# Kernel tuning notes

Hardware: AMD Instinct MI355X
Metric: run time of the kernel (lower is better)

Reference implementation:

```python
import jax, jax.numpy as jnp
import numpy as np

N_USERS = 100000
N_ITEMS = 50000
N_ENTITIES = 150000
N_EDGES = 2000000
NNZ = 1000000
CHANNEL = 64
N_HOPS = 2
TEMPERATURE = 0.2
PDIST_EPS = 1e-6   # torch.nn.PairwiseDistance default eps (added to the diff)
NORM_EPS = 1e-12   # F.normalize default eps


def setup_inputs() -> dict:
    key = jax.random.key(0)
    ks = jax.random.split(key, 8)
    return {
        "user_emb": jax.random.normal(ks[0], (N_USERS, CHANNEL), dtype=jnp.float32),
        "entity_emb": jax.random.normal(ks[1], (N_ENTITIES, CHANNEL), dtype=jnp.float32),
        "weight": jax.random.normal(ks[2], (20, CHANNEL), dtype=jnp.float32),
        "edge_index": jax.random.randint(ks[3], (2, N_EDGES), 0, N_ENTITIES, dtype=jnp.int64) if jax.config.jax_enable_x64 else jax.random.randint(ks[3], (2, N_EDGES), 0, N_ENTITIES, dtype=jnp.int32),
        "edge_type": jax.random.randint(ks[4], (N_EDGES,), 0, 20, dtype=jnp.int32),
        "inter_user": jax.random.randint(ks[5], (NNZ,), 0, N_USERS, dtype=jnp.int32),
        "inter_item": jax.random.randint(ks[6], (NNZ,), 0, N_ITEMS, dtype=jnp.int32),
        "inter_vals": jax.random.uniform(ks[7], (NNZ,), dtype=jnp.float32),
    }


def _l2_normalize(x):
    # F.normalize(x, p=2, dim=1): x / max(||x||, eps)
    n = jnp.sqrt(jnp.sum(x * x, axis=-1, keepdims=True))
    return x / jnp.maximum(n, NORM_EPS)


def _aggregate(entity_emb, head, tail, inter_user, inter_item, inter_vals):
    n_entities = entity_emb.shape[0]
    # scatter_mean over KG edges: mean of tail embeddings per head entity
    neigh = entity_emb[tail]                                   # [E, C]
    summed = jax.ops.segment_sum(neigh, head, num_segments=n_entities)
    cnt = jax.ops.segment_sum(jnp.ones((head.shape[0],), entity_emb.dtype), head,
                              num_segments=n_entities)
    entity_agg = summed / jnp.maximum(cnt, 1.0)[:, None]       # [n_entities, C]

    items = entity_agg[:N_ITEMS]                               # [n_items, C]
    g_items = items[inter_item]                                # [nnz, C]
    # user_mean = interact_map @ entity_agg[:n_items]  (sparse mm via segment_sum)
    user_mean = jax.ops.segment_sum(inter_vals[:, None] * g_items, inter_user,
                                    num_segments=N_USERS)      # [n_users, C]
    # pairwise L2 distance per interaction edge
    diff = g_items - user_mean[inter_user] + PDIST_EPS
    score = jnp.sqrt(jnp.sum(diff * diff, axis=-1)) / TEMPERATURE   # [nnz]
    # sparse softmax over each user row
    row_max = jax.ops.segment_max(score, inter_user, num_segments=N_USERS)
    e = jnp.exp(score - row_max[inter_user])
    denom = jax.ops.segment_sum(e, inter_user, num_segments=N_USERS)
    soft = e / denom[inter_user]                               # [nnz]
    # user_agg = soft_score_mat @ entity_agg[:n_items]
    user_agg = jax.ops.segment_sum(soft[:, None] * g_items, inter_user,
                                   num_segments=N_USERS)       # [n_users, C]
    return user_agg, entity_agg


def reference(user_emb, entity_emb, weight, edge_index, edge_type,
              inter_user, inter_item, inter_vals):
    # GraphConv.forward with mess_dropout=False, node_dropout=False (deterministic)
    head, tail = edge_index[0], edge_index[1]
    user_res, entity_res = user_emb, entity_emb
    u, ent = user_emb, entity_emb
    for _ in range(N_HOPS):
        u, ent = _aggregate(ent, head, tail, inter_user, inter_item, inter_vals)
        ent = _l2_normalize(ent)
        u = _l2_normalize(u)
        entity_res = entity_res + ent
        user_res = user_res + u
    return user_res, entity_res
```

## Files before the change

kernel.cpp:

```cpp
#include <hip/hip_runtime.h>

#define N_USERS   100000
#define N_ITEMS   50000
#define N_ENT     150000
#define N_EDGES   2000000
#define NNZ       1000000
#define CH        64

#define CB_SHIFT  9
#define CB_SIZE   512
#define NB_E      ((N_ENT   + CB_SIZE - 1) >> CB_SHIFT)
#define NB_U      ((N_USERS + CB_SIZE - 1) >> CB_SHIFT)
#define A_CHUNK   4096
#define UCACHE    32

#define NBLK_CNT   512
#define NBLK_CONV  ((N_ENT * 16 + 255) / 256)
#define NBLK_BS_E  ((N_EDGES + A_CHUNK - 1) / A_CHUNK)
#define NBLK_BS_U  ((NNZ + A_CHUNK - 1) / A_CHUNK)
#define GB_GATHER  (N_ENT / 4)
#define GB_USER    (N_USERS / 4)

typedef __fp16 h2v __attribute__((ext_vector_type(2)));

__device__ __forceinline__ h2v h2z() { h2v z = {(__fp16)0.f, (__fp16)0.f}; return z; }
__device__ __forceinline__ h2v pk(float a, float b) { return __builtin_amdgcn_cvt_pkrtz(a, b); }
__device__ __forceinline__ unsigned int h2u(h2v h) { return __builtin_bit_cast(unsigned int, h); }
__device__ __forceinline__ h2v u2h(unsigned int u) { return __builtin_bit_cast(h2v, u); }
__device__ __forceinline__ float fdot2f(h2v a, h2v b, float c) {
    return __builtin_amdgcn_fdot2(a, b, c, false);
}

template<int CTRL>
__device__ __forceinline__ float dpp_mov(float x) {
    return __builtin_bit_cast(float, __builtin_amdgcn_update_dpp(
        0, __builtin_bit_cast(int, x), CTRL, 0xF, 0xF, true));
}
template<int CTRL>
__device__ __forceinline__ unsigned dpp_mov_u(unsigned x) {
    return (unsigned)__builtin_amdgcn_update_dpp(0, (int)x, CTRL, 0xF, 0xF, true);
}
__device__ __forceinline__ float red8(float x) {
    x += dpp_mov<0xB1>(x);
    x += dpp_mov<0x4E>(x);
    x += dpp_mov<0x141>(x);
    return x;
}
__device__ __forceinline__ h2v grpadd8(h2v a) {
    return a + u2h(dpp_mov_u<0x128>(h2u(a)));
}


__device__ __forceinline__ void coarse_count_f(const int* __restrict__ key, int n,
                                               unsigned int* __restrict__ gcnt, int nb,
                                               unsigned int* h, int bid, int nblk) {
    for (int i = threadIdx.x; i < nb; i += blockDim.x) h[i] = 0;
    __syncthreads();
    for (int e = bid * blockDim.x + threadIdx.x; e < n; e += nblk * blockDim.x)
        atomicAdd(&h[key[e] >> CB_SHIFT], 1u);
    __syncthreads();
    for (int i = threadIdx.x; i < nb; i += blockDim.x)
        if (h[i]) atomicAdd(&gcnt[i], h[i]);
}

__global__ void build_p1(const int* __restrict__ head, const int* __restrict__ iu,
                         const float* __restrict__ entity_emb, uint2* __restrict__ E0,
                         unsigned int* __restrict__ cntE, unsigned int* __restrict__ cntU) {
    __shared__ unsigned int h[CB_SIZE];
    int bid = blockIdx.x;
    if (bid < NBLK_CNT) {
        coarse_count_f(head, N_EDGES, cntE, NB_E, h, bid, NBLK_CNT);
    } else if (bid < 2 * NBLK_CNT) {
        coarse_count_f(iu, NNZ, cntU, NB_U, h, bid - NBLK_CNT, NBLK_CNT);
    } else {
        int i = (bid - 2 * NBLK_CNT) * 256 + threadIdx.x;
        if (i < N_ENT * 16) {
            float4 a = ((const float4*)entity_emb)[i];
            E0[i] = make_uint2(h2u(pk(a.x, a.y)), h2u(pk(a.z, a.w)));
        }
    }
}

__device__ __forceinline__ void coarse_scan_f(const unsigned int* __restrict__ gcnt,
                                              unsigned int* __restrict__ base,
                                              unsigned int* __restrict__ cursor, int nb,
                                              unsigned int* s) {
    int t = threadIdx.x;
    unsigned int v = (t < nb) ? gcnt[t] : 0u;
    s[t] = v;
    __syncthreads();
    for (int off = 1; off < 512; off <<= 1) {
        unsigned int u = 0;
        if (t >= off) u = s[t - off];
        __syncthreads();
        if (t >= off) s[t] += u;
        __syncthreads();
    }
    if (t < nb) { base[t] = s[t] - v; cursor[t] = s[t] - v; }
    if (t == nb) base[t] = s[nb - 1];
}

__global__ void build_p2(const unsigned int* __restrict__ cntE, unsigned int* __restrict__ baseE,
                         unsigned int* __restrict__ curE,
                         const unsigned int* __restrict__ cntU, unsigned int* __restrict__ baseU,
                         unsigned int* __restrict__ curU) {
    __shared__ unsigned int s[512];
    if (blockIdx.x == 0) coarse_scan_f(cntE, baseE, curE, NB_E, s);
    else                 coarse_scan_f(cntU, baseU, curU, NB_U, s);
}

__device__ __forceinline__ void binscat_ent_f(const int* __restrict__ head,
                                              const int* __restrict__ tail,
                                              unsigned int* __restrict__ cursor,
                                              unsigned int* __restrict__ binned,
                                              unsigned int* h, unsigned int* bb, int bid) {
    int lo = bid * A_CHUNK;
    int hi = min(lo + A_CHUNK, N_EDGES);
    for (int i = threadIdx.x; i < NB_E; i += blockDim.x) h[i] = 0;
    __syncthreads();
    for (int e = lo + threadIdx.x; e < hi; e += blockDim.x)
        atomicAdd(&h[head[e] >> CB_SHIFT], 1u);
    __syncthreads();
    for (int i = threadIdx.x; i < NB_E; i += blockDim.x) {
        unsigned int c = h[i];
        bb[i] = c ? atomicAdd(&cursor[i], c) : 0u;
        h[i] = 0;
    }
    __syncthreads();
    for (int e = lo + threadIdx.x; e < hi; e += blockDim.x) {
        int hd = head[e];
        int b = hd >> CB_SHIFT;
        unsigned int r = atomicAdd(&h[b], 1u);
        unsigned int local = (unsigned int)hd & (CB_SIZE - 1);
        binned[bb[b] + r] = (local << 18) | (unsigned int)tail[e];
    }
}

__device__ __forceinline__ void binscat_user_f(const int* __restrict__ iu,
                                               const int* __restrict__ ii,
                                               const float* __restrict__ iv,
                                               unsigned int* __restrict__ cursor,
                                               unsigned int* __restrict__ binned,
                                               float* __restrict__ binnedv,
                                               unsigned int* h, unsigned int* bb, int bid) {
    int lo = bid * A_CHUNK;
    int hi = min(lo + A_CHUNK, NNZ);
    for (int i = threadIdx.x; i < NB_U; i += blockDim.x) h[i] = 0;
    __syncthreads();
    for (int e = lo + threadIdx.x; e < hi; e += blockDim.x)
        atomicAdd(&h[iu[e] >> CB_SHIFT], 1u);
    __syncthreads();
    for (int i = threadIdx.x; i < NB_U; i += blockDim.x) {
        unsigned int c = h[i];
        bb[i] = c ? atomicAdd(&cursor[i], c) : 0u;
        h[i] = 0;
    }
    __syncthreads();
    for (int e = lo + threadIdx.x; e < hi; e += blockDim.x) {
        int u = iu[e];
        int b = u >> CB_SHIFT;
        unsigned int r = atomicAdd(&h[b], 1u);
        unsigned int slot = bb[b] + r;
        unsigned int local = (unsigned int)u & (CB_SIZE - 1);
        binned[slot] = (local << 16) | (unsigned int)ii[e];
        binnedv[slot] = iv[e];
    }
}

__global__ void build_p3e(const int* __restrict__ head, const int* __restrict__ tail,
                          unsigned int* __restrict__ curE, unsigned int* __restrict__ binnedE) {
    __shared__ unsigned int h[NB_E];
    __shared__ unsigned int bb[NB_E];
    binscat_ent_f(head, tail, curE, binnedE, h, bb, blockIdx.x);
}

__device__ __forceinline__ void build_ent_f(const unsigned int* __restrict__ base,
                                            const unsigned int* __restrict__ binned,
                                            int* __restrict__ col,
                                            unsigned int* __restrict__ row_start,
                                            unsigned int* h, unsigned int* ex,
                                            unsigned int* pairs, int b) {
    unsigned int s0 = base[b], s1 = base[b + 1];
    int t = threadIdx.x;
    h[2 * t] = 0; h[2 * t + 1] = 0;
    __syncthreads();
    for (unsigned int j = s0 + t; j < s1; j += 256)
        atomicAdd(&h[binned[j] >> 18], 1u);
    __syncthreads();
    unsigned int a0 = h[2 * t], a1 = h[2 * t + 1];
    pairs[t] = a0 + a1;
    __syncthreads();
    for (int off = 1; off < 256; off <<= 1) {
        unsigned int u = 0;
        if (t >= off) u = pairs[t - off];
        __syncthreads();
        if (t >= off) pairs[t] += u;
        __syncthreads();
    }
    unsigned int pe = pairs[t] - (a0 + a1);
    ex[2 * t] = pe;
    ex[2 * t + 1] = pe + a0;
    __syncthreads();
    int keybase = b << CB_SHIFT;
    #pragma unroll
    for (int k = 0; k < 2; ++k) {
        int i = 2 * t + k;
        int key = keybase + i;
        if (key < N_ENT) row_start[key] = s0 + ex[i];
    }
    if (b == 0 && t == 0) row_start[N_ENT] = base[NB_E];
    __syncthreads();
    h[2 * t] = 0; h[2 * t + 1] = 0;
    __syncthreads();
    for (unsigned int j = s0 + t; j < s1; j += 256) {
        unsigned int p = binned[j];
        unsigned int local = p >> 18;
        unsigned int r = atomicAdd(&h[local], 1u);
        col[s0 + ex[local] + r] = (int)(p & 0x3FFFFu);
    }
}

__device__ __forceinline__ void build_user_f(const unsigned int* __restrict__ base,
                                             const unsigned int* __restrict__ binned,
                                             const float* __restrict__ binnedv,
                                             int2* __restrict__ upair,
                                             unsigned int* __restrict__ u_row_start,
                                             unsigned int* h, unsigned int* ex,
                                             unsigned int* pairs, int b) {
    unsigned int s0 = base[b], s1 = base[b + 1];
    int t = threadIdx.x;
    h[2 * t] = 0; h[2 * t + 1] = 0;
    __syncthreads();
    for (unsigned int j = s0 + t; j < s1; j += 256)
        atomicAdd(&h[binned[j] >> 16], 1u);
    __syncthreads();
    unsigned int a0 = h[2 * t], a1 = h[2 * t + 1];
    pairs[t] = a0 + a1;
    __syncthreads();
    for (int off = 1; off < 256; off <<= 1) {
        unsigned int u = 0;
        if (t >= off) u = pairs[t - off];
        __syncthreads();
        if (t >= off) pairs[t] += u;
        __syncthreads();
    }
    unsigned int pe = pairs[t] - (a0 + a1);
    ex[2 * t] = pe;
    ex[2 * t + 1] = pe + a0;
    __syncthreads();
    int keybase = b << CB_SHIFT;
    #pragma unroll
    for (int k = 0; k < 2; ++k) {
        int i = 2 * t + k;
        int key = keybase + i;
        if (key < N_USERS) u_row_start[key] = s0 + ex[i];
    }
    if (b == 0 && t == 0) u_row_start[N_USERS] = base[NB_U];
    __syncthreads();
    h[2 * t] = 0; h[2 * t + 1] = 0;
    __syncthreads();
    for (unsigned int j = s0 + t; j < s1; j += 256) {
        unsigned int p = binned[j];
        float v = binnedv[j];
        unsigned int local = p >> 16;
        unsigned int r = atomicAdd(&h[local], 1u);
        upair[s0 + ex[local] + r] = make_int2((int)(p & 0xFFFFu), __float_as_int(v));
    }
}

__global__ void build_p3u_p4e(const int* __restrict__ iu, const int* __restrict__ ii,
                              const float* __restrict__ iv, unsigned int* __restrict__ curU,
                              unsigned int* __restrict__ binnedU, float* __restrict__ binnedUV,
                              const unsigned int* __restrict__ baseE,
                              const unsigned int* __restrict__ binnedE,
                              int* __restrict__ col, unsigned int* __restrict__ row_start) {
    __shared__ unsigned int h[CB_SIZE];
    __shared__ unsigned int ex[CB_SIZE];
    __shared__ unsigned int pairs[256];
    if (blockIdx.x < NBLK_BS_U)
        binscat_user_f(iu, ii, iv, curU, binnedU, binnedUV, h, ex , blockIdx.x);
    else
        build_ent_f(baseE, binnedE, col, row_start, h, ex, pairs, blockIdx.x - NBLK_BS_U);
}


__device__ __forceinline__ void gather_fin_row(int row, int lane,
        const uint4* __restrict__ entb, const unsigned int* __restrict__ row_start,
        const int* __restrict__ col,
        uint4* __restrict__ ent_out, uint4* __restrict__ items_out,
        const float* __restrict__ base_ent, const uint4* __restrict__ v1tab,
        float* __restrict__ out_ent, int mode) {
    int grp = lane >> 3;
    int t   = lane & 7;
    unsigned int s0 = row_start[row];
    unsigned int s1 = row_start[row + 1];

    h2v a0 = h2z(), a1 = h2z(), a2 = h2z(), a3 = h2z();
    unsigned int j = s0 + grp;
    for (; j + 8 < s1; j += 16) {
        uint4 x0 = entb[(size_t)col[j]     * 8 + t];
        uint4 x1 = entb[(size_t)col[j + 8] * 8 + t];
        a0 += u2h(x0.x) + u2h(x1.x);
        a1 += u2h(x0.y) + u2h(x1.y);
        a2 += u2h(x0.z) + u2h(x1.z);
        a3 += u2h(x0.w) + u2h(x1.w);
    }
    if (j < s1) {
        uint4 x = entb[(size_t)col[j] * 8 + t];
        a0 += u2h(x.x); a1 += u2h(x.y); a2 += u2h(x.z); a3 += u2h(x.w);
    }
    a0 = grpadd8(a0); a1 = grpadd8(a1); a2 = grpadd8(a2); a3 = grpadd8(a3);
    #pragma unroll
    for (int m = 16; m <= 32; m <<= 1) {
        a0 += u2h(__shfl_xor(h2u(a0), m, 64));
        a1 += u2h(__shfl_xor(h2u(a1), m, 64));
        a2 += u2h(__shfl_xor(h2u(a2), m, 64));
        a3 += u2h(__shfl_xor(h2u(a3), m, 64));
    }
    float inv = 1.0f / fmaxf((float)(s1 - s0), 1.0f);
    float m0 = (float)a0[0] * inv, m1 = (float)a0[1] * inv;
    float m2 = (float)a1[0] * inv, m3 = (float)a1[1] * inv;
    float m4 = (float)a2[0] * inv, m5 = (float)a2[1] * inv;
    float m6 = (float)a3[0] * inv, m7 = (float)a3[1] * inv;

    float sq = m0*m0 + m1*m1 + m2*m2 + m3*m3 + m4*m4 + m5*m5 + m6*m6 + m7*m7;
    sq = red8(sq);
    float invn = 1.0f / fmaxf(sqrtf(sq), 1e-12f);

    if (grp == 0) {
        size_t o = (size_t)row * 8 + t;
        if (row < N_ITEMS)
            items_out[o] = make_uint4(h2u(pk(m0, m1)), h2u(pk(m2, m3)),
                                      h2u(pk(m4, m5)), h2u(pk(m6, m7)));
        if (mode == 0) {
            ent_out[o] = make_uint4(h2u(pk(m0*invn, m1*invn)), h2u(pk(m2*invn, m3*invn)),
                                    h2u(pk(m4*invn, m5*invn)), h2u(pk(m6*invn, m7*invn)));
        } else {
            size_t fo = (size_t)row * 16 + 2 * t;
            float4 c0 = ((const float4*)base_ent)[fo];
            float4 c1 = ((const float4*)base_ent)[fo + 1];
            uint4 v1 = v1tab[o];
            h2v p0 = u2h(v1.x), p1 = u2h(v1.y), p2 = u2h(v1.z), p3 = u2h(v1.w);
            ((float4*)out_ent)[fo]     = make_float4(c0.x + (float)p0[0] + m0*invn,
                                                     c0.y + (float)p0[1] + m1*invn,
                                                     c0.z + (float)p1[0] + m2*invn,
                                                     c0.w + (float)p1[1] + m3*invn);
            ((float4*)out_ent)[fo + 1] = make_float4(c1.x + (float)p2[0] + m4*invn,
                                                     c1.y + (float)p2[1] + m5*invn,
                                                     c1.z + (float)p3[0] + m6*invn,
                                                     c1.w + (float)p3[1] + m7*invn);
        }
    }
}

template<int NS>
__device__ __forceinline__ void user_fast_path(
        unsigned int s0, unsigned int deg, int grp, int t,
        const uint4* __restrict__ itemsb, const int2* __restrict__ up,
        float& l, h2v& ac0, h2v& ac1, h2v& ac2, h2v& ac3) {
    const float SC = 5.0f * 1.44269504f;
    uint4 r[NS];
    float vw[NS];
    #pragma unroll
    for (int k = 0; k < NS; ++k) {
        unsigned int slot = (unsigned int)grp + 8u * k;
        if (slot < deg) {
            int2 p = up[s0 + slot];
            r[k] = itemsb[(size_t)p.x * 8 + t];
            vw[k] = __int_as_float(p.y);
        } else {
            r[k] = make_uint4(0u, 0u, 0u, 0u);
            vw[k] = 0.0f;
        }
    }
    h2v um0 = h2z(), um1 = h2z(), um2 = h2z(), um3 = h2z();
    #pragma unroll
    for (int k = 0; k < NS; ++k) {
        h2v v2 = pk(vw[k], vw[k]);
        um0 += v2 * u2h(r[k].x); um1 += v2 * u2h(r[k].y);
        um2 += v2 * u2h(r[k].z); um3 += v2 * u2h(r[k].w);
    }
    um0 = grpadd8(um0); um1 = grpadd8(um1); um2 = grpadd8(um2); um3 = grpadd8(um3);
    #pragma unroll
    for (int m = 16; m <= 32; m <<= 1) {
        um0 += u2h(__shfl_xor(h2u(um0), m, 64));
        um1 += u2h(__shfl_xor(h2u(um1), m, 64));
        um2 += u2h(__shfl_xor(h2u(um2), m, 64));
        um3 += u2h(__shfl_xor(h2u(um3), m, 64));
    }
    float scv[NS];
    float mloc = -1e30f;
    #pragma unroll
    for (int k = 0; k < NS; ++k) {
        unsigned int slot = (unsigned int)grp + 8u * k;
        h2v d0 = u2h(r[k].x) - um0, d1 = u2h(r[k].y) - um1;
        h2v d2 = u2h(r[k].z) - um2, d3 = u2h(r[k].w) - um3;
        float sq = fdot2f(d3, d3, fdot2f(d2, d2, fdot2f(d1, d1, fdot2f(d0, d0, 0.0f))));
        sq = red8(sq);
        float sc = sqrtf(sq) * SC;
        scv[k] = (slot < deg) ? sc : -1e30f;
        mloc = fmaxf(mloc, scv[k]);
    }
    mloc = fmaxf(mloc, dpp_mov<0x128>(mloc));
    float M = fmaxf(mloc, __shfl_xor(mloc, 16, 64));
    M = fmaxf(M, __shfl_xor(M, 32, 64));
    #pragma unroll
    for (int k = 0; k < NS; ++k) {
        float e = exp2f(scv[k] - M);
        l += e;
        h2v e2 = pk(e, e);
        ac0 += e2 * u2h(r[k].x); ac1 += e2 * u2h(r[k].y);
        ac2 += e2 * u2h(r[k].z); ac3 += e2 * u2h(r[k].w);
    }
}

__device__ __forceinline__ void fused_user_row(int row, int lane, uint4 (*cw)[8],
        const uint4* __restrict__ itemsb, const unsigned int* __restrict__ u_row_start,
        const int2* __restrict__ up, const float* __restrict__ base_user,
        float* __restrict__ out_user) {
    int grp = lane >> 3;
    int t   = lane & 7;
    unsigned int s0 = u_row_start[row];
    unsigned int s1 = u_row_start[row + 1];
    unsigned int deg = s1 - s0;

    const float SC = 5.0f * 1.44269504f;
    float l = 0.0f;
    h2v ac0 = h2z(), ac1 = h2z(), ac2 = h2z(), ac3 = h2z();

    if (__builtin_expect(deg <= 16, 1)) {
        user_fast_path<2>(s0, deg, grp, t, itemsb, up, l, ac0, ac1, ac2, ac3);
    } else if (deg <= UCACHE) {
        user_fast_path<4>(s0, deg, grp, t, itemsb, up, l, ac0, ac1, ac2, ac3);
    } else {
        h2v um0 = h2z(), um1 = h2z(), um2 = h2z(), um3 = h2z();
        for (unsigned int j = s0 + grp; j < s1; j += 8) {
            int2 p = up[j];
            uint4 r = itemsb[(size_t)p.x * 8 + t];
            int slot = (int)(j - s0);
            if (slot < UCACHE) cw[slot][t] = r;
            float v = __int_as_float(p.y);
            h2v v2 = pk(v, v);
            um0 += v2 * u2h(r.x); um1 += v2 * u2h(r.y);
            um2 += v2 * u2h(r.z); um3 += v2 * u2h(r.w);
        }
        um0 = grpadd8(um0); um1 = grpadd8(um1); um2 = grpadd8(um2); um3 = grpadd8(um3);
        #pragma unroll
        for (int m = 16; m <= 32; m <<= 1) {
            um0 += u2h(__shfl_xor(h2u(um0), m, 64));
            um1 += u2h(__shfl_xor(h2u(um1), m, 64));
            um2 += u2h(__shfl_xor(h2u(um2), m, 64));
            um3 += u2h(__shfl_xor(h2u(um3), m, 64));
        }
        float m_run = -1e30f;
        for (unsigned int j = s0 + grp; j < s1; j += 8) {
            int slot = (int)(j - s0);
            uint4 r = (slot < UCACHE) ? cw[slot][t]
                                      : itemsb[(size_t)up[j].x * 8 + t];
            h2v d0 = u2h(r.x) - um0, d1 = u2h(r.y) - um1;
            h2v d2 = u2h(r.z) - um2, d3 = u2h(r.w) - um3;
            float sq = fdot2f(d3, d3, fdot2f(d2, d2, fdot2f(d1, d1, fdot2f(d0, d0, 0.0f))));
            sq = red8(sq);
            float sc = sqrtf(sq) * SC;
            if (sc > m_run) {
                float s = exp2f(m_run - sc);
                l *= s;
                h2v s2 = pk(s, s);
                ac0 *= s2; ac1 *= s2; ac2 *= s2; ac3 *= s2;
                m_run = sc;
            }
            float e = exp2f(sc - m_run);
            l += e;
            h2v e2 = pk(e, e);
            ac0 += e2 * u2h(r.x); ac1 += e2 * u2h(r.y);
            ac2 += e2 * u2h(r.z); ac3 += e2 * u2h(r.w);
        }
        float mx = fmaxf(m_run, dpp_mov<0x128>(m_run));
        float M = fmaxf(mx, __shfl_xor(mx, 16, 64));
        M = fmaxf(M, __shfl_xor(M, 32, 64));
        float wgt = (l > 0.0f) ? exp2f(m_run - M) : 0.0f;
        l *= wgt;
        h2v w2 = pk(wgt, wgt);
        ac0 *= w2; ac1 *= w2; ac2 *= w2; ac3 *= w2;
    }

    l = l + dpp_mov<0x128>(l);
    ac0 = grpadd8(ac0); ac1 = grpadd8(ac1); ac2 = grpadd8(ac2); ac3 = grpadd8(ac3);
    #pragma unroll
    for (int m = 16; m <= 32; m <<= 1) {
        l   += __shfl_xor(l, m, 64);
        ac0 += u2h(__shfl_xor(h2u(ac0), m, 64));
        ac1 += u2h(__shfl_xor(h2u(ac1), m, 64));
        ac2 += u2h(__shfl_xor(h2u(ac2), m, 64));
        ac3 += u2h(__shfl_xor(h2u(ac3), m, 64));
    }
    float invl = (l > 0.0f) ? (1.0f / l) : 0.0f;
    float u0 = (float)ac0[0] * invl, u1 = (float)ac0[1] * invl;
    float u2 = (float)ac1[0] * invl, u3 = (float)ac1[1] * invl;
    float u4 = (float)ac2[0] * invl, u5 = (float)ac2[1] * invl;
    float u6 = (float)ac3[0] * invl, u7 = (float)ac3[1] * invl;

    float sq2 = u0*u0 + u1*u1 + u2*u2 + u3*u3 + u4*u4 + u5*u5 + u6*u6 + u7*u7;
    sq2 = red8(sq2);
    float inv = 1.0f / fmaxf(sqrtf(sq2), 1e-12f);
    if (grp == 0) {
        size_t fo = (size_t)row * 16 + 2 * t;
        float4 c0 = ((const float4*)base_user)[fo];
        float4 c1 = ((const float4*)base_user)[fo + 1];
        ((float4*)out_user)[fo]     = make_float4(c0.x + u0*inv, c0.y + u1*inv,
                                                  c0.z + u2*inv, c0.w + u3*inv);
        ((float4*)out_user)[fo + 1] = make_float4(c1.x + u4*inv, c1.y + u5*inv,
                                                  c1.z + u6*inv, c1.w + u7*inv);
    }
}


__global__ void gf1_p4u_k(const uint4* __restrict__ E0,
                          const unsigned int* __restrict__ row_start,
                          const int* __restrict__ col,
                          uint4* __restrict__ E1, uint4* __restrict__ itemsA,
                          const unsigned int* __restrict__ baseU,
                          const unsigned int* __restrict__ binnedU,
                          const float* __restrict__ binnedUV,
                          int2* __restrict__ upair, unsigned int* __restrict__ u_row_start) {
    __shared__ unsigned int h[CB_SIZE];
    __shared__ unsigned int ex[CB_SIZE];
    __shared__ unsigned int pairs[256];
    int bid = blockIdx.x;
    if (bid < NB_U) {
        build_user_f(baseU, binnedU, binnedUV, upair, u_row_start, h, ex, pairs, bid);
    } else {
        int row  = (bid - NB_U) * 4 + (threadIdx.x >> 6);
        gather_fin_row(row, threadIdx.x & 63, E0, row_start, col, E1, itemsA,
                       nullptr, nullptr, nullptr, 0);
    }
}

__global__ void g2_u1_k(const uint4* __restrict__ entb,
                        const unsigned int* __restrict__ row_start,
                        const int* __restrict__ col,
                        uint4* __restrict__ items_out,
                        const float* __restrict__ entity_emb,
                        float* __restrict__ out_ent,
                        const uint4* __restrict__ itemsb1,
                        const unsigned int* __restrict__ u_row_start,
                        const int2* __restrict__ up,
                        const float* __restrict__ base_user,
                        float* __restrict__ out_user) {
    __shared__ uint4 cache[4][UCACHE][8];
    int bid = blockIdx.x;
    int g5 = bid / 5, r5 = bid - g5 * 5;
    int w    = threadIdx.x >> 6;
    int lane = threadIdx.x & 63;
    if (r5 < 3) {
        int row = (g5 * 3 + r5) * 4 + w;
        gather_fin_row(row, lane, entb, row_start, col, nullptr, items_out,
                       entity_emb, entb, out_ent, 1);
    } else {
        int row = (g5 * 2 + (r5 - 3)) * 4 + w;
        fused_user_row(row, lane, cache[w], itemsb1, u_row_start, up,
                       base_user, out_user);
    }
}

__global__ void fused_user_k(const uint4* __restrict__ itemsb,
                             const unsigned int* __restrict__ u_row_start,
                             const int2* __restrict__ up,
                             const float* __restrict__ base_user,
                             float* __restrict__ out_user) {
    __shared__ uint4 cache[4][UCACHE][8];
    int wave = (blockIdx.x * blockDim.x + threadIdx.x) >> 6;
    int w    = threadIdx.x >> 6;
    int lane = threadIdx.x & 63;
    if (wave >= N_USERS) return;
    fused_user_row(wave, lane, cache[w], itemsb, u_row_start, up, base_user, out_user);
}

extern "C" void kernel_launch(void* const* d_in, const int* in_sizes, int n_in,
                              void* d_out, int out_size, void* d_ws, size_t ws_size,
                              hipStream_t stream) {
    const float* user_emb   = (const float*)d_in[0];
    const float* entity_emb = (const float*)d_in[1];
    const int*   edge_index = (const int*)d_in[3];
    const int*   iu = (const int*)d_in[5];
    const int*   ii = (const int*)d_in[6];
    const float* iv = (const float*)d_in[7];

    float* out_user = (float*)d_out;
    float* out_ent  = out_user + (size_t)N_USERS * CH;

    uint4* E0     = (uint4*)d_ws;
    uint4* E1     = E0 + (size_t)N_ENT * 8;
    uint4* itemsA = E1 + (size_t)N_ENT * 8;
    uint4* itemsB = itemsA + (size_t)N_ITEMS * 8;
    int2*  upair  = (int2*)(itemsB + (size_t)N_ITEMS * 8);
    int*   col    = (int*)(upair + NNZ);
    unsigned int* row_start   = (unsigned int*)(col + N_EDGES);
    unsigned int* u_row_start = row_start + N_ENT + 1;
    unsigned int* cntE  = u_row_start + N_USERS + 1;
    unsigned int* cntU  = cntE + NB_E;
    unsigned int* baseE = cntU + NB_U;
    unsigned int* curE  = baseE + NB_E + 1;
    unsigned int* baseU = curE + NB_E;
    unsigned int* curU  = baseU + NB_U + 1;

    unsigned int* binnedE  = (unsigned int*)E1;
    unsigned int* binnedU  = (unsigned int*)out_user;
    float*        binnedUV = (float*)(binnedU + NNZ);

    const int* head = edge_index;
    const int* tail = edge_index + N_EDGES;

    (void)hipMemsetAsync(cntE, 0, (size_t)(NB_E + NB_U) * 4, stream);
    build_p1<<<2 * NBLK_CNT + NBLK_CONV, 256, 0, stream>>>(head, iu, entity_emb,
                                                           (uint2*)E0, cntE, cntU);
    build_p2<<<2, 512, 0, stream>>>(cntE, baseE, curE, cntU, baseU, curU);
    build_p3e<<<NBLK_BS_E, 256, 0, stream>>>(head, tail, curE, binnedE);
    build_p3u_p4e<<<NBLK_BS_U + NB_E, 256, 0, stream>>>(iu, ii, iv, curU, binnedU, binnedUV,
                                                        baseE, binnedE, col, row_start);

    gf1_p4u_k<<<NB_U + GB_GATHER, 256, 0, stream>>>(E0, row_start, col, E1, itemsA,
                                                    baseU, binnedU, binnedUV,
                                                    upair, u_row_start);

    g2_u1_k<<<GB_GATHER + GB_USER, 256, 0, stream>>>(E1, row_start, col, itemsB,
                                                     entity_emb, out_ent,
                                                     itemsA, u_row_start, upair,
                                                     user_emb, out_user);

    fused_user_k<<<GB_USER, 256, 0, stream>>>(itemsB, u_row_start, upair,
                                              out_user, out_user);
}
```

Baseline: 463.6 us.

## Map one entity row per 8-lane group instead of per wave in KG gather

The entity gather/mean/normalize step now gives each 8-lane group its own row, so a wave handles 8 rows instead of splitting one row's neighbours across 8 groups and reducing with shuffles. This removes the cross-group shuffle reduction and the idle lanes on low-degree rows, and cuts the gather block count by 8x. The interleaving of gather and user blocks in the fused second-hop kernel is rebalanced to 3:16 with bounds checks. Rows of different degree in one wave may cause divergence, and fewer lanes per row means less memory-level parallelism on high-degree rows.

Result: faster. 434.8 us (-6.2%).

```diff
diff --git a/kernel.cpp b/kernel.cpp
--- a/kernel.cpp
+++ b/kernel.cpp
@@ -18,8 +18,9 @@
 #define NBLK_CONV  ((N_ENT * 16 + 255) / 256)
 #define NBLK_BS_E  ((N_EDGES + A_CHUNK - 1) / A_CHUNK)
 #define NBLK_BS_U  ((NNZ + A_CHUNK - 1) / A_CHUNK)
-#define GB_GATHER  (N_ENT / 4)
+#define GB_G8      ((N_ENT + 31) / 32)
 #define GB_USER    (N_USERS / 4)
+#define G2U1_NG    1563
 
 typedef __fp16 h2v __attribute__((ext_vector_type(2)));
 
@@ -284,22 +285,21 @@
 }
 
 
-__device__ __forceinline__ void gather_fin_row(int row, int lane,
+__device__ __forceinline__ void gather_fin_row8(int row, int t, bool valid,
         const uint4* __restrict__ entb, const unsigned int* __restrict__ row_start,
         const int* __restrict__ col,
         uint4* __restrict__ ent_out, uint4* __restrict__ items_out,
         const float* __restrict__ base_ent, const uint4* __restrict__ v1tab,
         float* __restrict__ out_ent, int mode) {
-    int grp = lane >> 3;
-    int t   = lane & 7;
-    unsigned int s0 = row_start[row];
-    unsigned int s1 = row_start[row + 1];
+    unsigned int s0 = 0, s1 = 0;
+    if (valid) { s0 = row_start[row]; s1 = row_start[row + 1]; }
 
     h2v a0 = h2z(), a1 = h2z(), a2 = h2z(), a3 = h2z();
-    unsigned int j = s0 + grp;
-    for (; j + 8 < s1; j += 16) {
-        uint4 x0 = entb[(size_t)col[j]     * 8 + t];
-        uint4 x1 = entb[(size_t)col[j + 8] * 8 + t];
+    unsigned int j = s0;
+    for (; j + 1 < s1; j += 2) {
+        int c0 = col[j], c1 = col[j + 1];
+        uint4 x0 = entb[(size_t)c0 * 8 + t];
+        uint4 x1 = entb[(size_t)c1 * 8 + t];
         a0 += u2h(x0.x) + u2h(x1.x);
         a1 += u2h(x0.y) + u2h(x1.y);
         a2 += u2h(x0.z) + u2h(x1.z);
@@ -308,14 +308,6 @@
     if (j < s1) {
         uint4 x = entb[(size_t)col[j] * 8 + t];
         a0 += u2h(x.x); a1 += u2h(x.y); a2 += u2h(x.z); a3 += u2h(x.w);
-    }
-    a0 = grpadd8(a0); a1 = grpadd8(a1); a2 = grpadd8(a2); a3 = grpadd8(a3);
-    #pragma unroll
-    for (int m = 16; m <= 32; m <<= 1) {
-        a0 += u2h(__shfl_xor(h2u(a0), m, 64));
-        a1 += u2h(__shfl_xor(h2u(a1), m, 64));
-        a2 += u2h(__shfl_xor(h2u(a2), m, 64));
-        a3 += u2h(__shfl_xor(h2u(a3), m, 64));
     }
     float inv = 1.0f / fmaxf((float)(s1 - s0), 1.0f);
     float m0 = (float)a0[0] * inv, m1 = (float)a0[1] * inv;
@@ -327,29 +319,28 @@
     sq = red8(sq);
     float invn = 1.0f / fmaxf(sqrtf(sq), 1e-12f);
 
-    if (grp == 0) {
-        size_t o = (size_t)row * 8 + t;
-        if (row < N_ITEMS)
-            items_out[o] = make_uint4(h2u(pk(m0, m1)), h2u(pk(m2, m3)),
-                                      h2u(pk(m4, m5)), h2u(pk(m6, m7)));
-        if (mode == 0) {
-            ent_out[o] = make_uint4(h2u(pk(m0*invn, m1*invn)), h2u(pk(m2*invn, m3*invn)),
-                                    h2u(pk(m4*invn, m5*invn)), h2u(pk(m6*invn, m7*invn)));
-        } else {
-            size_t fo = (size_t)row * 16 + 2 * t;
-            float4 c0 = ((const float4*)base_ent)[fo];
-            float4 c1 = ((const float4*)base_ent)[fo + 1];
-            uint4 v1 = v1tab[o];
-            h2v p0 = u2h(v1.x), p1 = u2h(v1.y), p2 = u2h(v1.z), p3 = u2h(v1.w);
-            ((float4*)out_ent)[fo]     = make_float4(c0.x + (float)p0[0] + m0*invn,
-                                                     c0.y + (float)p0[1] + m1*invn,
-                                                     c0.z + (float)p1[0] + m2*invn,
-                                                     c0.w + (float)p1[1] + m3*invn);
-            ((float4*)out_ent)[fo + 1] = make_float4(c1.x + (float)p2[0] + m4*invn,
-                                                     c1.y + (float)p2[1] + m5*invn,
-                                                     c1.z + (float)p3[0] + m6*invn,
-                                                     c1.w + (float)p3[1] + m7*invn);
-        }
+    if (!valid) return;
+    size_t o = (size_t)row * 8 + t;
+    if (row < N_ITEMS)
+        items_out[o] = make_uint4(h2u(pk(m0, m1)), h2u(pk(m2, m3)),
+                                  h2u(pk(m4, m5)), h2u(pk(m6, m7)));
+    if (mode == 0) {
+        ent_out[o] = make_uint4(h2u(pk(m0*invn, m1*invn)), h2u(pk(m2*invn, m3*invn)),
+                                h2u(pk(m4*invn, m5*invn)), h2u(pk(m6*invn, m7*invn)));
+    } else {
+        size_t fo = (size_t)row * 16 + 2 * t;
+        float4 c0 = ((const float4*)base_ent)[fo];
+        float4 c1 = ((const float4*)base_ent)[fo + 1];
+        uint4 v1 = v1tab[o];
+        h2v p0 = u2h(v1.x), p1 = u2h(v1.y), p2 = u2h(v1.z), p3 = u2h(v1.w);
+        ((float4*)out_ent)[fo]     = make_float4(c0.x + (float)p0[0] + m0*invn,
+                                                 c0.y + (float)p0[1] + m1*invn,
+                                                 c0.z + (float)p1[0] + m2*invn,
+                                                 c0.w + (float)p1[1] + m3*invn);
+        ((float4*)out_ent)[fo + 1] = make_float4(c1.x + (float)p2[0] + m4*invn,
+                                                 c1.y + (float)p2[1] + m5*invn,
+                                                 c1.z + (float)p3[0] + m6*invn,
+                                                 c1.w + (float)p3[1] + m7*invn);
     }
 }
 
@@ -530,9 +521,10 @@
     if (bid < NB_U) {
         build_user_f(baseU, binnedU, binnedUV, upair, u_row_start, h, ex, pairs, bid);
     } else {
-        int row  = (bid - NB_U) * 4 + (threadIdx.x >> 6);
-        gather_fin_row(row, threadIdx.x & 63, E0, row_start, col, E1, itemsA,
-                       nullptr, nullptr, nullptr, 0);
+        int lane = threadIdx.x & 63;
+        int row = (bid - NB_U) * 32 + (threadIdx.x >> 6) * 8 + (lane >> 3);
+        gather_fin_row8(row, lane & 7, row < N_ENT, E0, row_start, col, E1, itemsA,
+                        nullptr, nullptr, nullptr, 0);
     }
 }
 
@@ -549,17 +541,20 @@
                         float* __restrict__ out_user) {
     __shared__ uint4 cache[4][UCACHE][8];
     int bid = blockIdx.x;
-    int g5 = bid / 5, r5 = bid - g5 * 5;
+    int g = bid / 19, r = bid - g * 19;
     int w    = threadIdx.x >> 6;
     int lane = threadIdx.x & 63;
-    if (r5 < 3) {
-        int row = (g5 * 3 + r5) * 4 + w;
-        gather_fin_row(row, lane, entb, row_start, col, nullptr, items_out,
-                       entity_emb, entb, out_ent, 1);
+    if (r < 3) {
+        int gb = g * 3 + r;
+        int row = gb * 32 + w * 8 + (lane >> 3);
+        gather_fin_row8(row, lane & 7, row < N_ENT, entb, row_start, col,
+                        nullptr, items_out, entity_emb, entb, out_ent, 1);
     } else {
-        int row = (g5 * 2 + (r5 - 3)) * 4 + w;
-        fused_user_row(row, lane, cache[w], itemsb1, u_row_start, up,
-                       base_user, out_user);
+        int idx = g * 16 + (r - 3);
+        int row = idx * 4 + w;
+        if (row < N_USERS)
+            fused_user_row(row, lane, cache[w], itemsb1, u_row_start, up,
+                           base_user, out_user);
     }
 }
 
@@ -619,14 +614,14 @@
     build_p3u_p4e<<<NBLK_BS_U + NB_E, 256, 0, stream>>>(iu, ii, iv, curU, binnedU, binnedUV,
                                                         baseE, binnedE, col, row_start);
 
-    gf1_p4u_k<<<NB_U + GB_GATHER, 256, 0, stream>>>(E0, row_start, col, E1, itemsA,
-                                                    baseU, binnedU, binnedUV,
-                                                    upair, u_row_start);
-
-    g2_u1_k<<<GB_GATHER + GB_USER, 256, 0, stream>>>(E1, row_start, col, itemsB,
-                                                     entity_emb, out_ent,
-                                                     itemsA, u_row_start, upair,
-                                                     user_emb, out_user);
+    gf1_p4u_k<<<NB_U + GB_G8, 256, 0, stream>>>(E0, row_start, col, E1, itemsA,
+                                                baseU, binnedU, binnedUV,
+                                                upair, u_row_start);
+
+    g2_u1_k<<<G2U1_NG * 19, 256, 0, stream>>>(E1, row_start, col, itemsB,
+                                              entity_emb, out_ent,
+                                              itemsA, u_row_start, upair,
+                                              user_emb, out_user);
 
     fused_user_k<<<GB_USER, 256, 0, stream>>>(itemsB, u_row_start, upair,
                                               out_user, out_user);
```
